# Optimization experiments

Hardware: AMD Instinct MI355X
Metric: run time of the kernel (lower is better)

The kernel has to match this reference:

```python
import jax, jax.numpy as jnp
import numpy as np
import math

D_MODEL = 1024
NUM_HEADS = 16
MAX_LEN = 2048
B, S = 2, 2048


def setup_inputs() -> dict:
    key = jax.random.key(0)
    ks = jax.random.split(key, 6)
    w_scale = 1.0 / math.sqrt(D_MODEL)  # ~xavier
    return {
        "x": jax.random.normal(ks[0], (B, S, D_MODEL), dtype=jnp.float32),
        "Wq": jax.random.normal(ks[1], (D_MODEL, D_MODEL), dtype=jnp.float32) * w_scale,
        "bq": jnp.zeros((D_MODEL,), dtype=jnp.float32),
        "Wk": jax.random.normal(ks[2], (D_MODEL, D_MODEL), dtype=jnp.float32) * w_scale,
        "bk": jnp.zeros((D_MODEL,), dtype=jnp.float32),
        "Wv": jax.random.normal(ks[3], (D_MODEL, D_MODEL), dtype=jnp.float32) * w_scale,
        "bv": jnp.zeros((D_MODEL,), dtype=jnp.float32),
        "Wo": jax.random.normal(ks[4], (D_MODEL, D_MODEL), dtype=jnp.float32) * w_scale,
        "bo": jnp.zeros((D_MODEL,), dtype=jnp.float32),
        "Er": jax.random.normal(ks[5], (MAX_LEN, D_MODEL // NUM_HEADS), dtype=jnp.float32),
    }


def reference(x, Wq, bq, Wk, bk, Wv, bv, Wo, bo, Er):
    Bsz, Sl, Dm = x.shape
    H = NUM_HEADS
    dqk = Dm // H

    def split_heads(z):
        # [B,S,D] -> [B,H,S,dqk]
        return z.reshape(Bsz, Sl, H, dqk).transpose(0, 2, 1, 3)

    Q = split_heads(x @ Wq.T + bq)
    K = split_heads(x @ Wk.T + bk)
    V = split_heads(x @ Wv.T + bv)

    Er_sl = Er[MAX_LEN - Sl:, :]  # [S, dqk]
    # Faithful to source: contract over d -> [B,H,S], unsqueeze last dim
    QEr = jnp.einsum('bhld,ld->bhl', Q, Er_sl)[..., None]  # [B,H,S,1]
    # skew(): pad left by 1 on last dim, reshape, drop first row
    padded = jnp.pad(QEr, ((0, 0), (0, 0), (0, 0), (1, 0)))  # [B,H,S,2]
    Srel = padded.reshape(Bsz, H, 2, Sl)[:, :, 1:, :]  # [B,H,1,S]

    QK_t = jnp.einsum('bhld,bhmd->bhlm', Q, K)  # [B,H,S,S]
    attn_scores = (QK_t + Srel) / math.sqrt(dqk)

    causal = jnp.tril(jnp.ones((Sl, Sl), dtype=bool))  # [S,S]
    attn_scores = jnp.where(causal[None, None], attn_scores, -jnp.inf)

    attn_probs = jax.nn.softmax(attn_scores, axis=-1)
    attn_out = jnp.einsum('bhlm,bhmd->bhld', attn_probs, V)  # [B,H,S,dqk]
    attn_out = attn_out.transpose(0, 2, 1, 3).reshape(Bsz, Sl, Dm)
    return attn_out @ Wo.T + bo  # dropout omitted (eval mode)
```

## Files before the change

kernel.cpp:

```cpp
#include <hip/hip_runtime.h>
#include <hip/hip_bf16.h>

#define D_MODEL 1024
#define NHEAD 16
#define DH 64
#define BSZ 2
#define SEQ 2048
#define MROWS (BSZ*SEQ)
#define SCL_Q 0.1803368801111204f
#define CHSZ 17408

typedef __attribute__((ext_vector_type(4))) float f32x4;
typedef __attribute__((ext_vector_type(8))) __bf16 bf16x8;
typedef __attribute__((ext_vector_type(8))) unsigned short u16x8;

__device__ __forceinline__ float b2f(unsigned short u) {
    union { unsigned int i; float f; } v; v.i = ((unsigned int)u) << 16; return v.f;
}
__device__ __forceinline__ unsigned short f2b(float f) {
    union { float f; unsigned int i; } v; v.f = f;
    unsigned int u = v.i;
    u += 0x7fffu + ((u >> 16) & 1u);
    return (unsigned short)(u >> 16);
}

#define GLDS16(gptr, lptr) \
    __builtin_amdgcn_global_load_lds((__attribute__((address_space(1))) void*)(gptr), \
                                     (__attribute__((address_space(3))) void*)(lptr), 16, 0, 0)

__global__ __launch_bounds__(256) void cvt5(
    const float* __restrict__ sx,
    const float* __restrict__ s1, const float* __restrict__ s2,
    const float* __restrict__ s3, const float* __restrict__ s4,
    unsigned short* __restrict__ dx,
    unsigned short* __restrict__ d1, unsigned short* __restrict__ d2,
    unsigned short* __restrict__ d3, unsigned short* __restrict__ d4)
{
    const int seg = blockIdx.y;
    const float* src; unsigned short* dst; int n4;
    if (seg == 0)      { src = sx; dst = dx; n4 = MROWS*D_MODEL/4; }
    else if (seg == 1) { src = s1; dst = d1; n4 = D_MODEL*D_MODEL/4; }
    else if (seg == 2) { src = s2; dst = d2; n4 = D_MODEL*D_MODEL/4; }
    else if (seg == 3) { src = s3; dst = d3; n4 = D_MODEL*D_MODEL/4; }
    else               { src = s4; dst = d4; n4 = D_MODEL*D_MODEL/4; }
    int i = blockIdx.x * 256 + threadIdx.x;
    int stride = gridDim.x * 256;
    for (; i < n4; i += stride) {
        float4 v = ((const float4*)src)[i];
        ushort4 o;
        o.x = f2b(v.x); o.y = f2b(v.y); o.z = f2b(v.z); o.w = f2b(v.w);
        ((ushort4*)dst)[i] = o;
    }
}

__global__ __launch_bounds__(256) void gemm_qkv(
    const unsigned short* __restrict__ X,
    const unsigned short* __restrict__ Wq, const unsigned short* __restrict__ Wk,
    const unsigned short* __restrict__ Wv,
    const float* __restrict__ bq, const float* __restrict__ bk, const float* __restrict__ bv,
    unsigned short* __restrict__ Qo, unsigned short* __restrict__ Ko, unsigned short* __restrict__ Vo)
{
    __shared__ unsigned short lsA[2][128*32];
    __shared__ unsigned short lsB[2][128*32];
    const int tid = threadIdx.x;
    const int z = blockIdx.z;
    const unsigned short* W = (z==0) ? Wq : (z==1) ? Wk : Wv;
    const float* bias = (z==0) ? bq : (z==1) ? bk : bv;
    unsigned short* Out = (z==0) ? Qo : (z==1) ? Ko : Vo;
    const int tM = blockIdx.y * 128;
    const int tN = blockIdx.x * 128;
    const int w = tid >> 6, lane = tid & 63;
    const int wr = w >> 1, wc = w & 1;
    const int lr = lane & 15, lk = lane >> 4;
    const f32x4 fz = {0.f, 0.f, 0.f, 0.f};
    f32x4 acc[4][4];
    #pragma unroll
    for (int m = 0; m < 4; m++)
        #pragma unroll
        for (int n = 0; n < 4; n++) acc[m][n] = fz;

    const int e0 = tid, e1 = 256 + tid;
    const int r0 = e0 >> 2, c0 = ((e0 & 3) ^ (r0 & 3)) * 8;
    const int r1 = e1 >> 2, c1 = ((e1 & 3) ^ (r1 & 3)) * 8;

#define GEMM_STAGE(buf, k0_) do { \
        GLDS16(X + (size_t)(tM + r0) * D_MODEL + (k0_) + c0, &lsA[buf][e0 * 8]); \
        GLDS16(X + (size_t)(tM + r1) * D_MODEL + (k0_) + c1, &lsA[buf][e1 * 8]); \
        GLDS16(W + (size_t)(tN + r0) * D_MODEL + (k0_) + c0, &lsB[buf][e0 * 8]); \
        GLDS16(W + (size_t)(tN + r1) * D_MODEL + (k0_) + c1, &lsB[buf][e1 * 8]); \
    } while (0)

    GEMM_STAGE(0, 0);
    __syncthreads();
    int cur = 0;
    for (int k0 = 0; k0 < D_MODEL; k0 += 32) {
        if (k0 + 32 < D_MODEL) GEMM_STAGE(cur ^ 1, k0 + 32);
        bf16x8 af[4], bfr[4];
        #pragma unroll
        for (int m = 0; m < 4; m++) {
            int row = wr*64 + m*16 + lr;
            af[m] = *(const bf16x8*)&lsA[cur][row*32 + ((lk ^ (row & 3)) * 8)];
        }
        #pragma unroll
        for (int n = 0; n < 4; n++) {
            int row = wc*64 + n*16 + lr;
            bfr[n] = *(const bf16x8*)&lsB[cur][row*32 + ((lk ^ (row & 3)) * 8)];
        }
        #pragma unroll
        for (int m = 0; m < 4; m++)
            #pragma unroll
            for (int n = 0; n < 4; n++)
                acc[m][n] = __builtin_amdgcn_mfma_f32_16x16x32_bf16(af[m], bfr[n], acc[m][n], 0, 0, 0);
        __syncthreads();
        cur ^= 1;
    }
#undef GEMM_STAGE
    const float qscl = (z == 0) ? SCL_Q : 1.0f;
    #pragma unroll
    for (int m = 0; m < 4; m++) {
        int ibase = tM + wr*64 + m*16 + lk*4;
        #pragma unroll
        for (int n = 0; n < 4; n++) {
            int j = tN + wc*64 + n*16 + lr;
            float bj = bias[j];
            int h = j >> 6, d = j & 63;
            #pragma unroll
            for (int r = 0; r < 4; r++) {
                int row = ibase + r;
                int b = row >> 11, s = row & 2047;
                Out[((size_t)(b*NHEAD + h) * SEQ + s) * DH + d] = f2b((acc[m][n][r] + bj) * qscl);
            }
        }
    }
}

__global__ __launch_bounds__(512) void gemm_out(
    const unsigned short* __restrict__ X, const unsigned short* __restrict__ W,
    const float* __restrict__ bias, float* __restrict__ Out)
{
    __shared__ unsigned short lsA[2][128*32];
    __shared__ unsigned short lsB[2][64*32];
    const int tid = threadIdx.x;
    const int tM = blockIdx.y * 128;
    const int tN = blockIdx.x * 64;
    const int w = tid >> 6, lane = tid & 63;
    const int wr = w >> 1, wc = w & 1;
    const int lr = lane & 15, lk = lane >> 4;
    const f32x4 fz = {0.f, 0.f, 0.f, 0.f};
    f32x4 acc[2][2];
    #pragma unroll
    for (int m = 0; m < 2; m++)
        #pragma unroll
        for (int n = 0; n < 2; n++) acc[m][n] = fz;

    const int ra = tid >> 2, ca = ((tid & 3) ^ (ra & 3)) * 8;
    const int eb = tid & 255;
    const int rb = eb >> 2, cb = ((eb & 3) ^ (rb & 3)) * 8;

#define OUT_STAGE(buf, k0_) do { \
        GLDS16(X + (size_t)(tM + ra) * D_MODEL + (k0_) + ca, &lsA[buf][tid * 8]); \
        if (tid < 256) GLDS16(W + (size_t)(tN + rb) * D_MODEL + (k0_) + cb, &lsB[buf][eb * 8]); \
    } while (0)

    OUT_STAGE(0, 0);
    __syncthreads();
    int cur = 0;
    for (int k0 = 0; k0 < D_MODEL; k0 += 32) {
        if (k0 + 32 < D_MODEL) OUT_STAGE(cur ^ 1, k0 + 32);
        bf16x8 af[2], bfr[2];
        #pragma unroll
        for (int m = 0; m < 2; m++) {
            int row = wr*32 + m*16 + lr;
            af[m] = *(const bf16x8*)&lsA[cur][row*32 + ((lk ^ (row & 3)) * 8)];
        }
        #pragma unroll
        for (int n = 0; n < 2; n++) {
            int row = wc*32 + n*16 + lr;
            bfr[n] = *(const bf16x8*)&lsB[cur][row*32 + ((lk ^ (row & 3)) * 8)];
        }
        #pragma unroll
        for (int m = 0; m < 2; m++)
            #pragma unroll
            for (int n = 0; n < 2; n++)
                acc[m][n] = __builtin_amdgcn_mfma_f32_16x16x32_bf16(af[m], bfr[n], acc[m][n], 0, 0, 0);
        __syncthreads();
        cur ^= 1;
    }
#undef OUT_STAGE
    #pragma unroll
    for (int m = 0; m < 2; m++) {
        int ibase = tM + wr*32 + m*16 + lk*4;
        #pragma unroll
        for (int n = 0; n < 2; n++) {
            int j = tN + wc*32 + n*16 + lr;
            float bj = bias[j];
            #pragma unroll
            for (int r = 0; r < 4; r++)
                Out[(size_t)(ibase + r) * D_MODEL + j] = acc[m][n][r] + bj;
        }
    }
}

__global__ __launch_bounds__(256) void vtrans(const unsigned short* __restrict__ V,
                                              unsigned short* __restrict__ Vt) {
    __shared__ unsigned short t[64][80];
    const int bh = blockIdx.y;
    const int s0 = blockIdx.x * 64;
    const int tid = threadIdx.x;
    #pragma unroll
    for (int i = 0; i < 2; i++) {
        int e = i*256 + tid;
        int r = e >> 3, c = e & 7;
        u16x8 v = *(const u16x8*)&V[((size_t)bh * SEQ + s0 + r) * DH + c*8];
        *(u16x8*)&t[r][c*8] = v;
    }
    __syncthreads();
    #pragma unroll
    for (int i = 0; i < 2; i++) {
        int e = i*256 + tid;
        int d = e >> 3, c = e & 7;
        u16x8 o;
        #pragma unroll
        for (int j = 0; j < 8; j++) o[j] = t[c*8 + j][d];
        *(u16x8*)&Vt[((size_t)bh * DH + d) * SEQ + s0 + c*8] = o;
    }
}

__global__ __launch_bounds__(256) void qer_k(const unsigned short* __restrict__ Q,
                                             const float* __restrict__ Er,
                                             float* __restrict__ qer) {
    int gw = blockIdx.x * 4 + (threadIdx.x >> 6);
    int lane = threadIdx.x & 63;
    int bh = gw >> 10;
    int l = 1024 + (gw & 1023);
    float p = b2f(Q[((size_t)bh * SEQ + l) * DH + lane]) * Er[l * DH + lane];
    #pragma unroll
    for (int m = 32; m >= 1; m >>= 1) p += __shfl_xor(p, m, 64);
    if (lane == 0) qer[(size_t)bh * SEQ + l] = p;
}

__global__ __launch_bounds__(256, 3) void attn_k(
    const unsigned short* __restrict__ Q, const unsigned short* __restrict__ Kg,
    const unsigned short* __restrict__ Vt, const float* __restrict__ qer,
    unsigned short* __restrict__ Om, char* __restrict__ part)
{
    __shared__ unsigned short lsK[2][64*64];
    __shared__ unsigned short lsV[2][64*64];
    __shared__ unsigned short lsP[128*64];
    const unsigned char tab[24] = {
        28, 24, 20, 16, 58, 51, 34,  8,
        62, 54, 46, 38, 59, 42, 35,  4,
        63, 55, 47, 39, 50, 43, 12,  0
    };
    const int id = blockIdx.x;
    const int bh = id & 31;
    const int v = tab[id >> 5];
    const int j = v >> 2;
    const bool split = (v >> 1) & 1;
    const int half = v & 1;
    const int kt0 = (split && half) ? (j + 1) : 0;
    const int ktN = (split && !half) ? (j + 1) : (2*j + 2);
    const int b = bh >> 4, h = bh & 15;
    const int tid = threadIdx.x;
    const int w = tid >> 6, lane = tid & 63;
    const int lr = lane & 15, lk = lane >> 4;
    const int q0 = w*32 + lr, q1 = q0 + 16;
    const int qrow0 = j*128 + q0, qrow1 = qrow0 + 16;
    const f32x4 fz = {0.f, 0.f, 0.f, 0.f};

    const unsigned short* Qr0 = Q + ((size_t)bh * SEQ + qrow0) * DH;
    const unsigned short* Qr1 = Q + ((size_t)bh * SEQ + qrow1) * DH;
    bf16x8 bqa0 = *(const bf16x8*)&Qr0[lk*8];
    bf16x8 bqa1 = *(const bf16x8*)&Qr0[32 + lk*8];
    bf16x8 bqb0 = *(const bf16x8*)&Qr1[lk*8];
    bf16x8 bqb1 = *(const bf16x8*)&Qr1[32 + lk*8];

    const int sr0 = tid >> 3,          sc0 = ((tid & 7) ^ (sr0 & 7)) * 8;
    const int sr1 = (256 + tid) >> 3,  sc1 = (((256 + tid) & 7) ^ (sr1 & 7)) * 8;
    const unsigned short* kst0 = Kg + ((size_t)bh * SEQ + kt0*64 + sr0) * DH + sc0;
    const unsigned short* kst1 = Kg + ((size_t)bh * SEQ + kt0*64 + sr1) * DH + sc1;
    const unsigned short* vst0 = Vt + ((size_t)bh * DH + sr0) * SEQ + kt0*64 + sc0;
    const unsigned short* vst1 = Vt + ((size_t)bh * DH + sr1) * SEQ + kt0*64 + sc1;
    const float* qb = qer + (size_t)bh * SEQ + 1024 + kt0*32 + lk*2;

#define ATTN_STAGE(buf) do { \
        GLDS16(kst0, &lsK[buf][tid * 8]);        kst0 += 64*DH; \
        GLDS16(kst1, &lsK[buf][(256+tid) * 8]);  kst1 += 64*DH; \
        GLDS16(vst0, &lsV[buf][tid * 8]);        vst0 += 64; \
        GLDS16(vst1, &lsV[buf][(256+tid) * 8]);  vst1 += 64; \
    } while (0)

    f32x4 o0[4], o1[4];
    #pragma unroll
    for (int df = 0; df < 4; df++) { o0[df] = fz; o1[df] = fz; }
    float lp0 = 0.0f, lp1 = 0.0f;

    ATTN_STAGE(0);
    __syncthreads();
    int cur = 0;

    for (int kt = kt0; kt < ktN; kt++) {
        float2 bv[4];
        #pragma unroll
        for (int kf = 0; kf < 4; kf++) bv[kf] = *(const float2*)(qb + kf*8);
        qb += 32;
        if (kt + 1 < ktN) ATTN_STAGE(cur ^ 1);
        float st[4][4], su[4][4];
        __builtin_amdgcn_s_setprio(1);
        #pragma unroll
        for (int kf = 0; kf < 4; kf++) {
            int row = kf*16 + lr;
            bf16x8 a0 = *(const bf16x8*)&lsK[cur][row*64 + ((lk ^ (row & 7)) * 8)];
            bf16x8 a1 = *(const bf16x8*)&lsK[cur][row*64 + (((4 + lk) ^ (row & 7)) * 8)];
            f32x4 zv = fz, yv = fz;
            zv = __builtin_amdgcn_mfma_f32_16x16x32_bf16(a0, bqa0, zv, 0, 0, 0);
            zv = __builtin_amdgcn_mfma_f32_16x16x32_bf16(a1, bqa1, zv, 0, 0, 0);
            yv = __builtin_amdgcn_mfma_f32_16x16x32_bf16(a0, bqb0, yv, 0, 0, 0);
            yv = __builtin_amdgcn_mfma_f32_16x16x32_bf16(a1, bqb1, yv, 0, 0, 0);
            st[kf][0] = zv[0];
            st[kf][1] = zv[1] + bv[kf].x;
            st[kf][2] = zv[2];
            st[kf][3] = zv[3] + bv[kf].y;
            su[kf][0] = yv[0];
            su[kf][1] = yv[1] + bv[kf].x;
            su[kf][2] = yv[2];
            su[kf][3] = yv[3] + bv[kf].y;
        }
        __builtin_amdgcn_s_setprio(0);
        if (kt >= 2*j) {
            #pragma unroll
            for (int kf = 0; kf < 4; kf++) {
                int kg0 = kt*64 + kf*16 + lk*4;
                #pragma unroll
                for (int r = 0; r < 4; r++) {
                    if (kg0 + r > qrow0) st[kf][r] = -3.0e38f;
                    if (kg0 + r > qrow1) su[kf][r] = -3.0e38f;
                }
            }
        }
        #pragma unroll
        for (int kf = 0; kf < 4; kf++) {
            float p0 = exp2f(st[kf][0]);
            float p1 = exp2f(st[kf][1]);
            float p2 = exp2f(st[kf][2]);
            float p3 = exp2f(st[kf][3]);
            lp0 += (p0 + p1) + (p2 + p3);
            union { __hip_bfloat162 h2[2]; unsigned long long u; } pk;
            pk.h2[0] = __float22bfloat162_rn(float2{p0, p1});
            pk.h2[1] = __float22bfloat162_rn(float2{p2, p3});
            *(unsigned long long*)&lsP[q0*64 + ((((kf<<2)|lk) ^ ((lr&7)<<1))<<2)] = pk.u;
            float s0 = exp2f(su[kf][0]);
            float s1 = exp2f(su[kf][1]);
            float s2 = exp2f(su[kf][2]);
            float s3 = exp2f(su[kf][3]);
            lp1 += (s0 + s1) + (s2 + s3);
            pk.h2[0] = __float22bfloat162_rn(float2{s0, s1});
            pk.h2[1] = __float22bfloat162_rn(float2{s2, s3});
            *(unsigned long long*)&lsP[q1*64 + ((((kf<<2)|lk) ^ ((lr&7)<<1))<<2)] = pk.u;
        }
        bf16x8 pa0 = *(const bf16x8*)&lsP[q0*64 + ((lk ^ (lr&7))<<3)];
        bf16x8 pa1 = *(const bf16x8*)&lsP[q0*64 + (((4+lk) ^ (lr&7))<<3)];
        bf16x8 pb0 = *(const bf16x8*)&lsP[q1*64 + ((lk ^ (lr&7))<<3)];
        bf16x8 pb1 = *(const bf16x8*)&lsP[q1*64 + (((4+lk) ^ (lr&7))<<3)];
        __builtin_amdgcn_s_setprio(1);
        #pragma unroll
        for (int df = 0; df < 4; df++) {
            int row = df*16 + lr;
            bf16x8 v0 = *(const bf16x8*)&lsV[cur][row*64 + ((lk ^ (row & 7)) * 8)];
            bf16x8 v1 = *(const bf16x8*)&lsV[cur][row*64 + (((4 + lk) ^ (row & 7)) * 8)];
            o0[df] = __builtin_amdgcn_mfma_f32_16x16x32_bf16(v0, pa0, o0[df], 0, 0, 0);
            o0[df] = __builtin_amdgcn_mfma_f32_16x16x32_bf16(v1, pa1, o0[df], 0, 0, 0);
            o1[df] = __builtin_amdgcn_mfma_f32_16x16x32_bf16(v0, pb0, o1[df], 0, 0, 0);
            o1[df] = __builtin_amdgcn_mfma_f32_16x16x32_bf16(v1, pb1, o1[df], 0, 0, 0);
        }
        __builtin_amdgcn_s_setprio(0);
        __syncthreads();
        cur ^= 1;
    }
#undef ATTN_STAGE
    float l0 = lp0 + __shfl_xor(lp0, 16, 64);
    l0 += __shfl_xor(l0, 32, 64);
    float l1 = lp1 + __shfl_xor(lp1, 16, 64);
    l1 += __shfl_xor(l1, 32, 64);
    if (split) {
        char* cb = part + (size_t)((bh*8 + (j - 8))*2 + half) * CHSZ;
        unsigned short* ob = (unsigned short*)cb;
        #pragma unroll
        for (int df = 0; df < 4; df++) {
            ushort4 ov;
            ov.x = f2b(o0[df][0]); ov.y = f2b(o0[df][1]);
            ov.z = f2b(o0[df][2]); ov.w = f2b(o0[df][3]);
            *(ushort4*)&ob[q0*64 + df*16 + lk*4] = ov;
            ov.x = f2b(o1[df][0]); ov.y = f2b(o1[df][1]);
            ov.z = f2b(o1[df][2]); ov.w = f2b(o1[df][3]);
            *(ushort4*)&ob[q1*64 + df*16 + lk*4] = ov;
        }
        float* ml = (float*)(cb + 16384);
        if (lk == 0) {
            ml[q0] = 0.0f; ml[128 + q0] = l0;
            ml[q1] = 0.0f; ml[128 + q1] = l1;
        }
    } else {
        float inv0 = 1.0f / l0, inv1 = 1.0f / l1;
        #pragma unroll
        for (int df = 0; df < 4; df++) {
            ushort4 ov;
            ov.x = f2b(o0[df][0] * inv0);
            ov.y = f2b(o0[df][1] * inv0);
            ov.z = f2b(o0[df][2] * inv0);
            ov.w = f2b(o0[df][3] * inv0);
            *(ushort4*)&Om[((size_t)(b * SEQ + qrow0)) * D_MODEL + h*64 + df*16 + lk*4] = ov;
            ov.x = f2b(o1[df][0] * inv1);
            ov.y = f2b(o1[df][1] * inv1);
            ov.z = f2b(o1[df][2] * inv1);
            ov.w = f2b(o1[df][3] * inv1);
            *(ushort4*)&Om[((size_t)(b * SEQ + qrow1)) * D_MODEL + h*64 + df*16 + lk*4] = ov;
        }
    }
}

__global__ __launch_bounds__(256) void attn_merge(const char* __restrict__ part,
                                                  unsigned short* __restrict__ Om)
{
    const int bh = blockIdx.x & 31, jj = blockIdx.x >> 5;
    const int b = bh >> 4, h = bh & 15, j = 8 + jj;
    const char* c0 = part + (size_t)((bh*8 + jj)*2) * CHSZ;
    const char* c1 = c0 + CHSZ;
    const unsigned short* o0 = (const unsigned short*)c0;
    const unsigned short* o1 = (const unsigned short*)c1;
    const float* ml0 = (const float*)(c0 + 16384);
    const float* ml1 = (const float*)(c1 + 16384);
    const int t = threadIdx.x;
    const int q = t >> 1, dh = (t & 1) * 32;
    float m0 = ml0[q], l0 = ml0[128 + q];
    float m1 = ml1[q], l1 = ml1[128 + q];
    float M = fmaxf(m0, m1);
    float w0 = exp2f(m0 - M), w1 = exp2f(m1 - M);
    float inv = 1.0f / (l0 * w0 + l1 * w1);
    w0 *= inv; w1 *= inv;
    unsigned short* dst = Om + ((size_t)(b*SEQ + j*128 + q)) * D_MODEL + h*64 + dh;
    #pragma unroll
    for (int i = 0; i < 4; i++) {
        u16x8 a = *(const u16x8*)&o0[q*64 + dh + i*8];
        u16x8 c = *(const u16x8*)&o1[q*64 + dh + i*8];
        u16x8 ov;
        #pragma unroll
        for (int r = 0; r < 8; r++)
            ov[r] = f2b(b2f(a[r])*w0 + b2f(c[r])*w1);
        *(u16x8*)&dst[i*8] = ov;
    }
}

extern "C" void kernel_launch(void* const* d_in, const int* in_sizes, int n_in,
                              void* d_out, int out_size, void* d_ws, size_t ws_size,
                              hipStream_t stream) {
    const float* x  = (const float*)d_in[0];
    const float* Wq = (const float*)d_in[1];
    const float* bq = (const float*)d_in[2];
    const float* Wk = (const float*)d_in[3];
    const float* bk = (const float*)d_in[4];
    const float* Wv = (const float*)d_in[5];
    const float* bv = (const float*)d_in[6];
    const float* Wo = (const float*)d_in[7];
    const float* bo = (const float*)d_in[8];
    const float* Er = (const float*)d_in[9];

    char* ws = (char*)d_ws;
    const size_t MB = 1024*1024;
    unsigned short* xb  = (unsigned short*)(ws);
    unsigned short* Wqb = (unsigned short*)(ws + 8*MB);
    unsigned short* Wkb = (unsigned short*)(ws + 10*MB);
    unsigned short* Wvb = (unsigned short*)(ws + 12*MB);
    unsigned short* Wob = (unsigned short*)(ws + 14*MB);
    unsigned short* Qb  = (unsigned short*)(ws + 16*MB);
    unsigned short* Kb  = (unsigned short*)(ws + 24*MB);
    unsigned short* Vb  = (unsigned short*)(ws + 32*MB);
    unsigned short* Vtb = (unsigned short*)(ws + 40*MB);
    float* qer          = (float*)(ws + 48*MB);
    char*  part         = (char*)(ws + 48*MB + 262144);

    cvt5<<<dim3(1024, 5), 256, 0, stream>>>(x, Wq, Wk, Wv, Wo, xb, Wqb, Wkb, Wvb, Wob);

    gemm_qkv<<<dim3(8, 32, 3), 256, 0, stream>>>(xb, Wqb, Wkb, Wvb, bq, bk, bv, Qb, Kb, Vb);
    vtrans<<<dim3(32, 32), 256, 0, stream>>>(Vb, Vtb);
    qer_k<<<8192, 256, 0, stream>>>(Qb, Er, qer);
    attn_k<<<768, 256, 0, stream>>>(Qb, Kb, Vtb, qer, xb, part);
    attn_merge<<<256, 256, 0, stream>>>(part, xb);
    gemm_out<<<dim3(16, 32), 512, 0, stream>>>(xb, Wob, bo, (float*)d_out);
}
```

Baseline: 130.7 us.

## Rebalance causal attention with finer multi-way KV splits and n-way merge

Replaces the 2-way split schedule for the longest query tiles with a 40-entry table that splits the later query blocks into 2-4 KV chunks of roughly equal size, raising the grid from 768 to 1280 workgroups. Partial outputs go to slots scattered across workspace regions that are no longer needed at that point (the x and Wq copies, V, and the tail region), and the merge kernel now sums a variable number of chunks. The merge drops the max-rescale because the partial results already use a shared max (the stored max was always zero). The goal is to shorten the critical-path workgroup and reduce tail imbalance, at the cost of more partial writes, more merge traffic, and reuse of workspace buffers that must not be needed later.

```diff
diff --git a/kernel.cpp b/kernel.cpp
--- a/kernel.cpp
+++ b/kernel.cpp
@@ -8,7 +8,7 @@
 #define SEQ 2048
 #define MROWS (BSZ*SEQ)
 #define SCL_Q 0.1803368801111204f
-#define CHSZ 17408
+#define CHSZ2 16896
 
 typedef __attribute__((ext_vector_type(4))) float f32x4;
 typedef __attribute__((ext_vector_type(8))) __bf16 bf16x8;
@@ -22,6 +22,13 @@
     unsigned int u = v.i;
     u += 0x7fffu + ((u >> 16) & 1u);
     return (unsigned short)(u >> 16);
+}
+
+__device__ __forceinline__ char* slotptr(char* wsb, int s) {
+    const size_t MB = 1024*1024;
+    if (s < 372)  return wsb + 8*MB            + (size_t)s * CHSZ2;
+    if (s < 868)  return wsb + 32*MB           + (size_t)(s - 372) * CHSZ2;
+    return              wsb + 48*MB + 262144   + (size_t)(s - 868) * CHSZ2;
 }
 
 #define GLDS16(gptr, lptr) \
@@ -242,24 +249,30 @@
 __global__ __launch_bounds__(256, 3) void attn_k(
     const unsigned short* __restrict__ Q, const unsigned short* __restrict__ Kg,
     const unsigned short* __restrict__ Vt, const float* __restrict__ qer,
-    unsigned short* __restrict__ Om, char* __restrict__ part)
+    unsigned short* __restrict__ Om, char* __restrict__ wsb)
 {
     __shared__ unsigned short lsK[2][64*64];
     __shared__ unsigned short lsV[2][64*64];
     __shared__ unsigned short lsP[128*64];
-    const unsigned char tab[24] = {
-        28, 24, 20, 16, 58, 51, 34,  8,
-        62, 54, 46, 38, 59, 42, 35,  4,
-        63, 55, 47, 39, 50, 43, 12,  0
-    };
+    const unsigned char jt[40]  = {15,15,15,15,14,14,11,11,11,10, 7, 7, 3,
+                                   14,14,13,13,13,13,12,12,10,10, 9, 9, 6, 6,
+                                   12,12, 9, 8, 8, 8, 5, 5, 2, 4, 4, 1, 0};
+    const unsigned char k0t[40] = { 0, 8,16,24, 0, 8, 0, 8,16, 0, 0, 8, 0,
+                                   16,23, 0, 7,14,21, 0, 7, 8,15, 0, 7, 0, 7,
+                                   14,20,14, 0, 6,12, 0, 6, 0, 0, 5, 0, 0};
+    const unsigned char k1t[40] = { 8,16,24,32, 8,16, 8,16,24, 8, 8,16, 8,
+                                   23,30, 7,14,21,28, 7,14,15,22, 7,14, 7,14,
+                                   20,26,20, 6,12,18, 6,12, 6, 5,10, 4, 2};
+    const unsigned char st40[40]= {32,33,34,35,28,29,17,18,19,14, 6, 7,255,
+                                   30,31,24,25,26,27,20,21,15,16,11,12, 4, 5,
+                                   22,23,13, 8, 9,10, 2, 3,255, 0, 1,255,255};
     const int id = blockIdx.x;
     const int bh = id & 31;
-    const int v = tab[id >> 5];
-    const int j = v >> 2;
-    const bool split = (v >> 1) & 1;
-    const int half = v & 1;
-    const int kt0 = (split && half) ? (j + 1) : 0;
-    const int ktN = (split && !half) ? (j + 1) : (2*j + 2);
+    const int u = id >> 5;
+    const int j = jt[u];
+    const int kt0 = k0t[u];
+    const int ktN = k1t[u];
+    const int sl = st40[u];
     const int b = bh >> 4, h = bh & 15;
     const int tid = threadIdx.x;
     const int w = tid >> 6, lane = tid & 63;
@@ -382,8 +395,8 @@
     l0 += __shfl_xor(l0, 32, 64);
     float l1 = lp1 + __shfl_xor(lp1, 16, 64);
     l1 += __shfl_xor(l1, 32, 64);
-    if (split) {
-        char* cb = part + (size_t)((bh*8 + (j - 8))*2 + half) * CHSZ;
+    if (sl != 255) {
+        char* cb = slotptr(wsb, bh*36 + sl);
         unsigned short* ob = (unsigned short*)cb;
         #pragma unroll
         for (int df = 0; df < 4; df++) {
@@ -395,11 +408,8 @@
             ov.z = f2b(o1[df][2]); ov.w = f2b(o1[df][3]);
             *(ushort4*)&ob[q1*64 + df*16 + lk*4] = ov;
         }
-        float* ml = (float*)(cb + 16384);
-        if (lk == 0) {
-            ml[q0] = 0.0f; ml[128 + q0] = l0;
-            ml[q1] = 0.0f; ml[128 + q1] = l1;
-        }
+        float* lv = (float*)(cb + 16384);
+        if (lk == 0) { lv[q0] = l0; lv[q1] = l1; }
     } else {
         float inv0 = 1.0f / l0, inv1 = 1.0f / l1;
         #pragma unroll
@@ -419,34 +429,40 @@
     }
 }
 
-__global__ __launch_bounds__(256) void attn_merge(const char* __restrict__ part,
+__global__ __launch_bounds__(256) void attn_merge(char* __restrict__ wsb,
                                                   unsigned short* __restrict__ Om)
 {
+    const unsigned char offt[12] = {0,2,4,6,8,11,14,17,20,24,28,32};
+    const unsigned char nct[12]  = {2,2,2,2,3,3,3,3,4,4,4,4};
     const int bh = blockIdx.x & 31, jj = blockIdx.x >> 5;
-    const int b = bh >> 4, h = bh & 15, j = 8 + jj;
-    const char* c0 = part + (size_t)((bh*8 + jj)*2) * CHSZ;
-    const char* c1 = c0 + CHSZ;
-    const unsigned short* o0 = (const unsigned short*)c0;
-    const unsigned short* o1 = (const unsigned short*)c1;
-    const float* ml0 = (const float*)(c0 + 16384);
-    const float* ml1 = (const float*)(c1 + 16384);
+    const int b = bh >> 4, h = bh & 15, j = 4 + jj;
+    const int nc = nct[jj];
+    const int base = bh*36 + offt[jj];
     const int t = threadIdx.x;
     const int q = t >> 1, dh = (t & 1) * 32;
-    float m0 = ml0[q], l0 = ml0[128 + q];
-    float m1 = ml1[q], l1 = ml1[128 + q];
-    float M = fmaxf(m0, m1);
-    float w0 = exp2f(m0 - M), w1 = exp2f(m1 - M);
-    float inv = 1.0f / (l0 * w0 + l1 * w1);
-    w0 *= inv; w1 *= inv;
+    float acc[32];
+    #pragma unroll
+    for (int i = 0; i < 32; i++) acc[i] = 0.f;
+    float lsum = 0.f;
+    for (int c = 0; c < nc; c++) {
+        const char* cb = slotptr(wsb, base + c);
+        const unsigned short* ob = (const unsigned short*)cb;
+        const float* lv = (const float*)(cb + 16384);
+        lsum += lv[q];
+        #pragma unroll
+        for (int i = 0; i < 4; i++) {
+            u16x8 a = *(const u16x8*)&ob[q*64 + dh + i*8];
+            #pragma unroll
+            for (int r = 0; r < 8; r++) acc[i*8 + r] += b2f(a[r]);
+        }
+    }
+    float inv = 1.0f / lsum;
     unsigned short* dst = Om + ((size_t)(b*SEQ + j*128 + q)) * D_MODEL + h*64 + dh;
     #pragma unroll
     for (int i = 0; i < 4; i++) {
-        u16x8 a = *(const u16x8*)&o0[q*64 + dh + i*8];
-        u16x8 c = *(const u16x8*)&o1[q*64 + dh + i*8];
         u16x8 ov;
         #pragma unroll
-        for (int r = 0; r < 8; r++)
-            ov[r] = f2b(b2f(a[r])*w0 + b2f(c[r])*w1);
+        for (int r = 0; r < 8; r++) ov[r] = f2b(acc[i*8 + r] * inv);
         *(u16x8*)&dst[i*8] = ov;
     }
 }
@@ -477,14 +493,13 @@
     unsigned short* Vb  = (unsigned short*)(ws + 32*MB);
     unsigned short* Vtb = (unsigned short*)(ws + 40*MB);
     float* qer          = (float*)(ws + 48*MB);
-    char*  part         = (char*)(ws + 48*MB + 262144);
 
     cvt5<<<dim3(1024, 5), 256, 0, stream>>>(x, Wq, Wk, Wv, Wo, xb, Wqb, Wkb, Wvb, Wob);
 
     gemm_qkv<<<dim3(8, 32, 3), 256, 0, stream>>>(xb, Wqb, Wkb, Wvb, bq, bk, bv, Qb, Kb, Vb);
     vtrans<<<dim3(32, 32), 256, 0, stream>>>(Vb, Vtb);
     qer_k<<<8192, 256, 0, stream>>>(Qb, Er, qer);
-    attn_k<<<768, 256, 0, stream>>>(Qb, Kb, Vtb, qer, xb, part);
-    attn_merge<<<256, 256, 0, stream>>>(part, xb);
+    attn_k<<<1280, 256, 0, stream>>>(Qb, Kb, Vtb, qer, xb, ws);
+    attn_merge<<<384, 256, 0, stream>>>(ws, xb);
     gemm_out<<<dim3(16, 32), 512, 0, stream>>>(xb, Wob, bo, (float*)d_out);
 }
```

Result: faster. 123.4 us (-5.6%).
